# Kernel optimization log

Hardware: AMD Instinct MI355X
Metric: run time of the kernel (lower is better)

Reference implementation:

```python
import math
import jax, jax.numpy as jnp
import numpy as np

B, S, E = 4, 2048, 1024

def setup_inputs() -> dict:
    key = jax.random.key(0)
    k1, k2, k3 = jax.random.split(key, 3)
    X = jax.random.normal(k1, (B, S, E), dtype=jnp.float32)
    # nn.Linear(E, 3E): weight [3E, E], bias [3E]; scale weights for sane softmax
    W = jax.random.normal(k2, (3 * E, E), dtype=jnp.float32) * (1.0 / math.sqrt(E))
    b = jax.random.normal(k3, (3 * E,), dtype=jnp.float32) * 0.01
    return {"X": X, "W": W, "b": b}

def reference(X, W, b):
    E_ = X.shape[-1]
    # fused QKV projection: X @ W^T + b -> [B, S, 3E]
    qkv = jnp.einsum('bse,fe->bsf', X, W) + b
    q, k, v = jnp.split(qkv, 3, axis=-1)
    scores = jnp.einsum('bqe,bke->bqk', q, k) / math.sqrt(E_)
    attention_weight = jax.nn.softmax(scores, axis=-1)  # [B, S, S]
    output = jnp.einsum('bqk,bke->bqe', attention_weight, v)
    return (output, attention_weight)
```

## Files before the change

kernel.cpp:

```cpp
#include <hip/hip_runtime.h>
#include <math.h>

typedef __bf16 bf16;
typedef __bf16 bf16x4 __attribute__((ext_vector_type(4)));
typedef __bf16 bf16x8 __attribute__((ext_vector_type(8)));
typedef float f32x4 __attribute__((ext_vector_type(4)));

#define MODE_QKV    0
#define MODE_SCORES 1
#define MODE_PV     2

__device__ inline void gload_lds16(const bf16* g, bf16* l) {
    __builtin_amdgcn_global_load_lds(
        (const __attribute__((address_space(1))) void*)g,
        (__attribute__((address_space(3))) void*)l, 16, 0, 0);
}

template <int MODE>
__global__ __launch_bounds__(256) void mfma_nt(
    const bf16* __restrict__ A, const bf16* __restrict__ B,
    const float* __restrict__ bias, void* __restrict__ Cv,
    int K, int lda, int ldb, int ldc,
    long sA, long sB, long sC, float alpha)
{
    A += (long)blockIdx.z * sA;
    B += (long)blockIdx.z * sB;

    __shared__ bf16 As[128 * 32] __attribute__((aligned(16)));
    __shared__ bf16 Bs[128 * 32] __attribute__((aligned(16)));

    const int t  = threadIdx.x;
    const int m0 = blockIdx.y * 128;
    const int n0 = blockIdx.x * 128;

    const int lane = t & 63;
    const int wave = t >> 6;
    const int wrow = (wave >> 1) * 64;
    const int wcol = (wave & 1) * 64;
    const int fr   = lane & 15;
    const int kq8  = lane >> 4;

    const int r0 = t >> 2,         q0 = t & 3;
    const int r1 = (t + 256) >> 2, q1 = (t + 256) & 3;
    const int k80 = (q0 ^ ((r0 >> 1) & 3)) * 8;
    const int k81 = (q1 ^ ((r1 >> 1) & 3)) * 8;

    f32x4 acc[4][4] = {};

    for (int k0 = 0; k0 < K; k0 += 32) {
        gload_lds16(A + (long)(m0 + r0) * lda + k0 + k80, &As[t * 8]);
        gload_lds16(A + (long)(m0 + r1) * lda + k0 + k81, &As[(t + 256) * 8]);
        gload_lds16(B + (long)(n0 + r0) * ldb + k0 + k80, &Bs[t * 8]);
        gload_lds16(B + (long)(n0 + r1) * ldb + k0 + k81, &Bs[(t + 256) * 8]);
        __syncthreads();

        bf16x8 af[4], bfr[4];
#pragma unroll
        for (int i = 0; i < 4; i++) {
            const int ra = wrow + i * 16 + fr;
            const int rb = wcol + i * 16 + fr;
            af[i]  = *(const bf16x8*)&As[(ra * 4 + (kq8 ^ ((ra >> 1) & 3))) * 8];
            bfr[i] = *(const bf16x8*)&Bs[(rb * 4 + (kq8 ^ ((rb >> 1) & 3))) * 8];
        }
#pragma unroll
        for (int i = 0; i < 4; i++)
#pragma unroll
            for (int j = 0; j < 4; j++)
                acc[i][j] = __builtin_amdgcn_mfma_f32_16x16x32_bf16(
                    af[i], bfr[j], acc[i][j], 0, 0, 0);
        __syncthreads();
    }

    const int r4 = (lane >> 4) * 4;
    if constexpr (MODE == MODE_PV) {
        float* C = (float*)Cv + (long)blockIdx.z * sC;
#pragma unroll
        for (int j = 0; j < 4; j++) {
            const int col = n0 + wcol + j * 16 + fr;
#pragma unroll
            for (int i = 0; i < 4; i++)
#pragma unroll
                for (int r = 0; r < 4; r++) {
                    const long row = m0 + wrow + i * 16 + r4 + r;
                    C[row * ldc + col] = acc[i][j][r];
                }
        }
    } else {
        bf16* C = (bf16*)Cv + (long)blockIdx.z * sC;
#pragma unroll
        for (int j = 0; j < 4; j++) {
            const int col = n0 + wcol + j * 16 + fr;
            const float bv = (MODE == MODE_QKV) ? bias[col] : 0.f;
#pragma unroll
            for (int i = 0; i < 4; i++)
#pragma unroll
                for (int r = 0; r < 4; r++) {
                    const long row = m0 + wrow + i * 16 + r4 + r;
                    float v = acc[i][j][r];
                    if constexpr (MODE == MODE_QKV)
                        C[row * ldc + col] = (bf16)(v + bv);
                    else
                        C[row * ldc + col] = (bf16)__expf(alpha * v);
                }
        }
    }
}

__global__ __launch_bounds__(256) void f32_to_bf16(
    const float* __restrict__ in, bf16* __restrict__ out, long n)
{
    long i = ((long)blockIdx.x * 256 + threadIdx.x) * 4;
    if (i < n) {
        float4 v = *(const float4*)(in + i);
        bf16x4 o = { (bf16)v.x, (bf16)v.y, (bf16)v.z, (bf16)v.w };
        *(bf16x4*)(out + i) = o;
    }
}

__global__ __launch_bounds__(256) void transpose_v(
    const bf16* __restrict__ V, bf16* __restrict__ Vt)
{
    __shared__ bf16 tile[32][33];
    const bf16* Vb  = V  + (long)blockIdx.z * 2048 * 3072;
    bf16*       Vtb = Vt + (long)blockIdx.z * 1024 * 2048;
    const int s0 = blockIdx.x * 32, e0 = blockIdx.y * 32;
    const int tx = threadIdx.x & 31, ty = threadIdx.x >> 5;
#pragma unroll
    for (int i = 0; i < 32; i += 8)
        tile[ty + i][tx] = Vb[(long)(s0 + ty + i) * 3072 + e0 + tx];
    __syncthreads();
#pragma unroll
    for (int i = 0; i < 32; i += 8)
        Vtb[(long)(e0 + ty + i) * 2048 + s0 + tx] = tile[tx][ty + i];
}

__global__ __launch_bounds__(256) void norm_rows(
    bf16* __restrict__ Pu, float* __restrict__ out1)
{
    bf16* p  = Pu   + (long)blockIdx.x * 2048;
    float* o = out1 + (long)blockIdx.x * 2048;
    const int t = threadIdx.x;
    bf16x8 v = *(const bf16x8*)(p + t * 8);
    float f[8];
    float s = 0.f;
#pragma unroll
    for (int k = 0; k < 8; k++) { f[k] = (float)v[k]; s += f[k]; }
#pragma unroll
    for (int off = 32; off > 0; off >>= 1) s += __shfl_xor(s, off);
    __shared__ float red[4];
    const int wid = t >> 6, lane = t & 63;
    if (lane == 0) red[wid] = s;
    __syncthreads();
    s = red[0] + red[1] + red[2] + red[3];
    const float inv = 1.0f / s;
    float4 a, b;
    a.x = f[0] * inv; a.y = f[1] * inv; a.z = f[2] * inv; a.w = f[3] * inv;
    b.x = f[4] * inv; b.y = f[5] * inv; b.z = f[6] * inv; b.w = f[7] * inv;
    *(float4*)(o + t * 8)     = a;
    *(float4*)(o + t * 8 + 4) = b;
    bf16x8 w;
#pragma unroll
    for (int k = 0; k < 8; k++) w[k] = (bf16)(f[k] * inv);
    *(bf16x8*)(p + t * 8) = w;
}

extern "C" void kernel_launch(void* const* d_in, const int* in_sizes, int n_in,
                              void* d_out, int out_size, void* d_ws, size_t ws_size,
                              hipStream_t stream)
{
    const int B = 4, S = 2048, E = 1024;
    const float* X    = (const float*)d_in[0];
    const float* W    = (const float*)d_in[1];
    const float* bias = (const float*)d_in[2];

    float* out0 = (float*)d_out;
    float* out1 = out0 + (long)B * S * E;

    char* ws = (char*)d_ws;
    bf16* qkvb = (bf16*)(ws);
    bf16* Vt   = (bf16*)(ws + 50331648);
    bf16* Pu   = (bf16*)(ws + 67108864);
    bf16* Xb   = (bf16*)(ws + 67108864);
    bf16* Wb   = (bf16*)(ws + 83886080);

    f32_to_bf16<<<(long)B * S * E / 1024, 256, 0, stream>>>(X, Xb, (long)B * S * E);
    f32_to_bf16<<<(long)3 * E * E / 1024, 256, 0, stream>>>(W, Wb, (long)3 * E * E);

    mfma_nt<MODE_QKV><<<dim3(3 * E / 128, B * S / 128, 1), 256, 0, stream>>>(
        Xb, Wb, bias, qkvb, E, E, E, 3 * E, 0, 0, 0, 1.0f);

    transpose_v<<<dim3(S / 32, E / 32, B), 256, 0, stream>>>(qkvb + 2 * E, Vt);

    mfma_nt<MODE_SCORES><<<dim3(S / 128, S / 128, B), 256, 0, stream>>>(
        qkvb, qkvb + E, nullptr, Pu, E, 3 * E, 3 * E, S,
        (long)S * 3 * E, (long)S * 3 * E, (long)S * S, 0.03125f);

    norm_rows<<<B * S, 256, 0, stream>>>(Pu, out1);

    mfma_nt<MODE_PV><<<dim3(E / 128, S / 128, B), 256, 0, stream>>>(
        Pu, Vt, nullptr, out0, S, S, S, E,
        (long)S * S, (long)E * S, (long)S * E, 1.0f);
}
```

Baseline: 346.7 us.

## Rework GEMM kernel into 8-wave 256-row tiles with 4-stage LDS pipeline

Replaces the 4-wave 128x128 GEMM with an 8-wave kernel using 256-row tiles (256 or 128 columns) and a 4-deep ring of LDS buffers filled by async global-to-LDS loads issued three tiles ahead. Loads are interleaved with MFMA phases behind explicit vmcnt waits and barriers, and setprio raises wave priority during MFMA bursts. The aim is to hide global-memory latency and increase data reuse per tile. The cost is much more LDS and more accumulator registers per thread, which lowers occupancy and makes correctness depend on hand-tuned wait counts.

```diff
diff --git a/kernel.cpp b/kernel.cpp
--- a/kernel.cpp
+++ b/kernel.cpp
@@ -16,87 +16,154 @@
         (__attribute__((address_space(3))) void*)l, 16, 0, 0);
 }
 
-template <int MODE>
-__global__ __launch_bounds__(256) void mfma_nt(
+template <int MODE, int BN>
+__global__ __launch_bounds__(512) void mfma_nt8(
     const bf16* __restrict__ A, const bf16* __restrict__ B,
     const float* __restrict__ bias, void* __restrict__ Cv,
     int K, int lda, int ldb, int ldc,
     long sA, long sB, long sC, float alpha)
 {
+    constexpr int BM  = 256, BK = 32;
+    constexpr int WN  = BN / 4;
+    constexpr int NJ  = WN / 16;
+    constexpr int LB  = (BN == 256) ? 2 : 1;
+    constexpr int LPT = 2 + LB;
+
     A += (long)blockIdx.z * sA;
     B += (long)blockIdx.z * sB;
 
-    __shared__ bf16 As[128 * 32] __attribute__((aligned(16)));
-    __shared__ bf16 Bs[128 * 32] __attribute__((aligned(16)));
-
-    const int t  = threadIdx.x;
-    const int m0 = blockIdx.y * 128;
-    const int n0 = blockIdx.x * 128;
-
+    __shared__ bf16 As[4 * BM * BK] __attribute__((aligned(16)));
+    __shared__ bf16 Bs[4 * BN * BK] __attribute__((aligned(16)));
+
+    const int t    = threadIdx.x;
+    const int m0   = blockIdx.y * BM;
+    const int n0   = blockIdx.x * BN;
     const int lane = t & 63;
     const int wave = t >> 6;
-    const int wrow = (wave >> 1) * 64;
-    const int wcol = (wave & 1) * 64;
+    const int wr   = (wave >> 2) * 128;
+    const int wc   = (wave & 3) * WN;
     const int fr   = lane & 15;
     const int kq8  = lane >> 4;
 
-    const int r0 = t >> 2,         q0 = t & 3;
-    const int r1 = (t + 256) >> 2, q1 = (t + 256) & 3;
-    const int k80 = (q0 ^ ((r0 >> 1) & 3)) * 8;
-    const int k81 = (q1 ^ ((r1 >> 1) & 3)) * 8;
-
-    f32x4 acc[4][4] = {};
-
-    for (int k0 = 0; k0 < K; k0 += 32) {
-        gload_lds16(A + (long)(m0 + r0) * lda + k0 + k80, &As[t * 8]);
-        gload_lds16(A + (long)(m0 + r1) * lda + k0 + k81, &As[(t + 256) * 8]);
-        gload_lds16(B + (long)(n0 + r0) * ldb + k0 + k80, &Bs[t * 8]);
-        gload_lds16(B + (long)(n0 + r1) * ldb + k0 + k81, &Bs[(t + 256) * 8]);
-        __syncthreads();
-
-        bf16x8 af[4], bfr[4];
-#pragma unroll
-        for (int i = 0; i < 4; i++) {
-            const int ra = wrow + i * 16 + fr;
-            const int rb = wcol + i * 16 + fr;
-            af[i]  = *(const bf16x8*)&As[(ra * 4 + (kq8 ^ ((ra >> 1) & 3))) * 8];
-            bfr[i] = *(const bf16x8*)&Bs[(rb * 4 + (kq8 ^ ((rb >> 1) & 3))) * 8];
-        }
+    const int ra0 = t >> 2,         qa0 = t & 3;
+    const int ra1 = (t + 512) >> 2, qa1 = (t + 512) & 3;
+    const int ga0 = (qa0 ^ ((ra0 >> 1) & 3)) * 8;
+    const int ga1 = (qa1 ^ ((ra1 >> 1) & 3)) * 8;
+
+    const bf16* gA0 = A + (long)(m0 + ra0) * lda + ga0;
+    const bf16* gA1 = A + (long)(m0 + ra1) * lda + ga1;
+    const bf16* gB0 = B + (long)(n0 + ra0) * ldb + ga0;
+    const bf16* gB1 = B + (long)(n0 + ((LB == 2) ? ra1 : ra0)) * ldb
+                        + ((LB == 2) ? ga1 : ga0);
+
+    int offA[8], offB[NJ];
+#pragma unroll
+    for (int i = 0; i < 8; i++) {
+        const int r = wr + i * 16 + fr;
+        offA[i] = (r * 4 + (kq8 ^ ((r >> 1) & 3))) * 8;
+    }
+#pragma unroll
+    for (int j = 0; j < NJ; j++) {
+        const int r = wc + j * 16 + fr;
+        offB[j] = (r * 4 + (kq8 ^ ((r >> 1) & 3))) * 8;
+    }
+
+    const int NT = K / BK;
+
+#define STAGE_A(tt) do {                                                   \
+    const int  _s = (tt) & 3; const long _k = (long)(tt) * BK;             \
+    gload_lds16(gA0 + _k, &As[_s * BM * BK + t * 8]);                      \
+    gload_lds16(gA1 + _k, &As[_s * BM * BK + (t + 512) * 8]);              \
+} while (0)
+
+#define STAGE_B(tt) do {                                                   \
+    const int  _s = (tt) & 3; const long _k = (long)(tt) * BK;             \
+    gload_lds16(gB0 + _k, &Bs[_s * BN * BK + t * 8]);                      \
+    if constexpr (LB == 2)                                                 \
+        gload_lds16(gB1 + _k, &Bs[_s * BN * BK + (t + 512) * 8]);          \
+} while (0)
+
+    f32x4 acc[8][NJ] = {};
+
+    STAGE_A(0); STAGE_B(0);
+    STAGE_A(1); STAGE_B(1);
+    STAGE_A(2); STAGE_B(2);
+    asm volatile("s_waitcnt vmcnt(%0)" :: "i"(2 * LPT) : "memory");
+    __builtin_amdgcn_s_barrier();
+
+    for (int tt = 0; tt < NT; ++tt) {
+        const bf16* as = &As[(tt & 3) * BM * BK];
+        const bf16* bs = &Bs[(tt & 3) * BN * BK];
+        bf16x8 af[4], bfr[NJ];
+
+        if (tt + 3 < NT) STAGE_A(tt + 3);
+#pragma unroll
+        for (int i = 0; i < 4; i++) af[i] = *(const bf16x8*)&as[offA[i]];
+#pragma unroll
+        for (int j = 0; j < NJ; j++) bfr[j] = *(const bf16x8*)&bs[offB[j]];
+        asm volatile("" ::: "memory");
+        __builtin_amdgcn_s_barrier();
+        __builtin_amdgcn_s_setprio(1);
 #pragma unroll
         for (int i = 0; i < 4; i++)
 #pragma unroll
-            for (int j = 0; j < 4; j++)
+            for (int j = 0; j < NJ; j++)
                 acc[i][j] = __builtin_amdgcn_mfma_f32_16x16x32_bf16(
                     af[i], bfr[j], acc[i][j], 0, 0, 0);
-        __syncthreads();
-    }
+        __builtin_amdgcn_s_setprio(0);
+        asm volatile("" ::: "memory");
+        __builtin_amdgcn_s_barrier();
+
+        if (tt + 3 < NT) STAGE_B(tt + 3);
+#pragma unroll
+        for (int i = 0; i < 4; i++) af[i] = *(const bf16x8*)&as[offA[4 + i]];
+        asm volatile("" ::: "memory");
+        __builtin_amdgcn_s_barrier();
+        __builtin_amdgcn_s_setprio(1);
+#pragma unroll
+        for (int i = 0; i < 4; i++)
+#pragma unroll
+            for (int j = 0; j < NJ; j++)
+                acc[4 + i][j] = __builtin_amdgcn_mfma_f32_16x16x32_bf16(
+                    af[i], bfr[j], acc[4 + i][j], 0, 0, 0);
+        __builtin_amdgcn_s_setprio(0);
+        if (tt < NT - 3)
+            asm volatile("s_waitcnt vmcnt(%0)" :: "i"(2 * LPT) : "memory");
+        else if (tt == NT - 3)
+            asm volatile("s_waitcnt vmcnt(%0)" :: "i"(LPT) : "memory");
+        else if (tt == NT - 2)
+            asm volatile("s_waitcnt vmcnt(0)" ::: "memory");
+        __builtin_amdgcn_s_barrier();
+    }
+#undef STAGE_A
+#undef STAGE_B
 
     const int r4 = (lane >> 4) * 4;
     if constexpr (MODE == MODE_PV) {
         float* C = (float*)Cv + (long)blockIdx.z * sC;
 #pragma unroll
-        for (int j = 0; j < 4; j++) {
-            const int col = n0 + wcol + j * 16 + fr;
-#pragma unroll
-            for (int i = 0; i < 4; i++)
+        for (int j = 0; j < NJ; j++) {
+            const int col = n0 + wc + j * 16 + fr;
+#pragma unroll
+            for (int I = 0; I < 8; I++)
 #pragma unroll
                 for (int r = 0; r < 4; r++) {
-                    const long row = m0 + wrow + i * 16 + r4 + r;
-                    C[row * ldc + col] = acc[i][j][r];
+                    const long row = m0 + wr + I * 16 + r4 + r;
+                    C[row * ldc + col] = acc[I][j][r];
                 }
         }
     } else {
         bf16* C = (bf16*)Cv + (long)blockIdx.z * sC;
 #pragma unroll
-        for (int j = 0; j < 4; j++) {
-            const int col = n0 + wcol + j * 16 + fr;
+        for (int j = 0; j < NJ; j++) {
+            const int col = n0 + wc + j * 16 + fr;
             const float bv = (MODE == MODE_QKV) ? bias[col] : 0.f;
 #pragma unroll
-            for (int i = 0; i < 4; i++)
+            for (int I = 0; I < 8; I++)
 #pragma unroll
                 for (int r = 0; r < 4; r++) {
-                    const long row = m0 + wrow + i * 16 + r4 + r;
-                    float v = acc[i][j][r];
+                    const long row = m0 + wr + I * 16 + r4 + r;
+                    float v = acc[I][j][r];
                     if constexpr (MODE == MODE_QKV)
                         C[row * ldc + col] = (bf16)(v + bv);
                     else
@@ -186,18 +253,18 @@
     f32_to_bf16<<<(long)B * S * E / 1024, 256, 0, stream>>>(X, Xb, (long)B * S * E);
     f32_to_bf16<<<(long)3 * E * E / 1024, 256, 0, stream>>>(W, Wb, (long)3 * E * E);
 
-    mfma_nt<MODE_QKV><<<dim3(3 * E / 128, B * S / 128, 1), 256, 0, stream>>>(
+    mfma_nt8<MODE_QKV, 128><<<dim3(3 * E / 128, B * S / 256, 1), 512, 0, stream>>>(
         Xb, Wb, bias, qkvb, E, E, E, 3 * E, 0, 0, 0, 1.0f);
 
     transpose_v<<<dim3(S / 32, E / 32, B), 256, 0, stream>>>(qkvb + 2 * E, Vt);
 
-    mfma_nt<MODE_SCORES><<<dim3(S / 128, S / 128, B), 256, 0, stream>>>(
+    mfma_nt8<MODE_SCORES, 256><<<dim3(S / 256, S / 256, B), 512, 0, stream>>>(
         qkvb, qkvb + E, nullptr, Pu, E, 3 * E, 3 * E, S,
         (long)S * 3 * E, (long)S * 3 * E, (long)S * S, 0.03125f);
 
     norm_rows<<<B * S, 256, 0, stream>>>(Pu, out1);
 
-    mfma_nt<MODE_PV><<<dim3(E / 128, S / 128, B), 256, 0, stream>>>(
+    mfma_nt8<MODE_PV, 128><<<dim3(E / 128, S / 256, B), 512, 0, stream>>>(
         Pu, Vt, nullptr, out0, S, S, S, E,
         (long)S * S, (long)E * S, (long)S * E, 1.0f);
 }
```

Result: slower. 362.0 us (+4.4%).

## Triple-buffer GEMM LDS tiles with async prefetch and split MFMA waits

Applied to the files above, without the earlier changes.

Replaces the single-buffered load, sync, compute loop in the shared GEMM kernel with a three-slot LDS ring. Tile k+2 is prefetched via global_load_lds while tile k is computed, with explicit vmcnt/lgkmcnt waits and one barrier per iteration. LDS reads are issued as inline ds_read_b128 and the MFMAs are split into two halves, so the first half can start before all fragments arrive. Wave priority is raised around the MFMA blocks. The cost is three times the LDS per block, which may lower occupancy, and correctness now relies on hand-placed waitcnt values that the compiler does not check.

```diff
diff --git a/kernel.cpp b/kernel.cpp
--- a/kernel.cpp
+++ b/kernel.cpp
@@ -14,6 +14,14 @@
     __builtin_amdgcn_global_load_lds(
         (const __attribute__((address_space(1))) void*)g,
         (__attribute__((address_space(3))) void*)l, 16, 0, 0);
+}
+
+__device__ inline bf16x8 ds_read16(const bf16* p) {
+    bf16x8 r;
+    asm volatile("ds_read_b128 %0, %1"
+        : "=v"(r)
+        : "v"((const __attribute__((address_space(3))) bf16*)p));
+    return r;
 }
 
 template <int MODE>
@@ -23,11 +31,13 @@
     int K, int lda, int ldb, int ldc,
     long sA, long sB, long sC, float alpha)
 {
+    constexpr int SLOT = 128 * 32;
+
     A += (long)blockIdx.z * sA;
     B += (long)blockIdx.z * sB;
 
-    __shared__ bf16 As[128 * 32] __attribute__((aligned(16)));
-    __shared__ bf16 Bs[128 * 32] __attribute__((aligned(16)));
+    __shared__ bf16 As[3 * SLOT] __attribute__((aligned(16)));
+    __shared__ bf16 Bs[3 * SLOT] __attribute__((aligned(16)));
 
     const int t  = threadIdx.x;
     const int m0 = blockIdx.y * 128;
@@ -45,31 +55,88 @@
     const int k80 = (q0 ^ ((r0 >> 1) & 3)) * 8;
     const int k81 = (q1 ^ ((r1 >> 1) & 3)) * 8;
 
+    const bf16* gA0 = A + (long)(m0 + r0) * lda + k80;
+    const bf16* gA1 = A + (long)(m0 + r1) * lda + k81;
+    const bf16* gB0 = B + (long)(n0 + r0) * ldb + k80;
+    const bf16* gB1 = B + (long)(n0 + r1) * ldb + k81;
+
+    int offA[4], offB[4];
+#pragma unroll
+    for (int i = 0; i < 4; i++) {
+        const int ra = wrow + i * 16 + fr;
+        const int rb = wcol + i * 16 + fr;
+        offA[i] = (ra * 4 + (kq8 ^ ((ra >> 1) & 3))) * 8;
+        offB[i] = (rb * 4 + (kq8 ^ ((rb >> 1) & 3))) * 8;
+    }
+
+    const int NT = K / 32;
+
+#define STAGE(tt_, ss_) do {                                               \
+    const long _k = (long)(tt_) * 32;                                      \
+    bf16* _as = &As[(ss_) * SLOT];                                         \
+    bf16* _bs = &Bs[(ss_) * SLOT];                                         \
+    gload_lds16(gA0 + _k, _as + t * 8);                                    \
+    gload_lds16(gA1 + _k, _as + (t + 256) * 8);                            \
+    gload_lds16(gB0 + _k, _bs + t * 8);                                    \
+    gload_lds16(gB1 + _k, _bs + (t + 256) * 8);                            \
+} while (0)
+
     f32x4 acc[4][4] = {};
 
-    for (int k0 = 0; k0 < K; k0 += 32) {
-        gload_lds16(A + (long)(m0 + r0) * lda + k0 + k80, &As[t * 8]);
-        gload_lds16(A + (long)(m0 + r1) * lda + k0 + k81, &As[(t + 256) * 8]);
-        gload_lds16(B + (long)(n0 + r0) * ldb + k0 + k80, &Bs[t * 8]);
-        gload_lds16(B + (long)(n0 + r1) * ldb + k0 + k81, &Bs[(t + 256) * 8]);
-        __syncthreads();
+    STAGE(0, 0);
+    STAGE(1, 1);
+    asm volatile("s_waitcnt vmcnt(4)" ::: "memory");
+    __builtin_amdgcn_s_barrier();
+
+    int cs = 0;
+    for (int tt = 0; tt < NT; ++tt) {
+        const int ss = (cs >= 1) ? cs - 1 : 2;
+        if (tt + 2 < NT) STAGE(tt + 2, ss);
+
+        const bf16* as = &As[cs * SLOT];
+        const bf16* bs = &Bs[cs * SLOT];
 
         bf16x8 af[4], bfr[4];
-#pragma unroll
-        for (int i = 0; i < 4; i++) {
-            const int ra = wrow + i * 16 + fr;
-            const int rb = wcol + i * 16 + fr;
-            af[i]  = *(const bf16x8*)&As[(ra * 4 + (kq8 ^ ((ra >> 1) & 3))) * 8];
-            bfr[i] = *(const bf16x8*)&Bs[(rb * 4 + (kq8 ^ ((rb >> 1) & 3))) * 8];
-        }
-#pragma unroll
-        for (int i = 0; i < 4; i++)
+        af[0]  = ds_read16(as + offA[0]);
+        af[1]  = ds_read16(as + offA[1]);
+        bfr[0] = ds_read16(bs + offB[0]);
+        bfr[1] = ds_read16(bs + offB[1]);
+        bfr[2] = ds_read16(bs + offB[2]);
+        bfr[3] = ds_read16(bs + offB[3]);
+        af[2]  = ds_read16(as + offA[2]);
+        af[3]  = ds_read16(as + offA[3]);
+
+        asm volatile("s_waitcnt lgkmcnt(2)" ::: "memory");
+        __builtin_amdgcn_sched_barrier(0);
+        __builtin_amdgcn_s_setprio(1);
+#pragma unroll
+        for (int i = 0; i < 2; i++)
 #pragma unroll
             for (int j = 0; j < 4; j++)
                 acc[i][j] = __builtin_amdgcn_mfma_f32_16x16x32_bf16(
                     af[i], bfr[j], acc[i][j], 0, 0, 0);
-        __syncthreads();
-    }
+        __builtin_amdgcn_s_setprio(0);
+
+        asm volatile("s_waitcnt lgkmcnt(0)" ::: "memory");
+        __builtin_amdgcn_sched_barrier(0);
+        __builtin_amdgcn_s_setprio(1);
+#pragma unroll
+        for (int i = 2; i < 4; i++)
+#pragma unroll
+            for (int j = 0; j < 4; j++)
+                acc[i][j] = __builtin_amdgcn_mfma_f32_16x16x32_bf16(
+                    af[i], bfr[j], acc[i][j], 0, 0, 0);
+        __builtin_amdgcn_s_setprio(0);
+
+        if (tt + 2 < NT)
+            asm volatile("s_waitcnt vmcnt(4)" ::: "memory");
+        else
+            asm volatile("s_waitcnt vmcnt(0)" ::: "memory");
+        __builtin_amdgcn_s_barrier();
+
+        cs = (cs < 2) ? cs + 1 : 0;
+    }
+#undef STAGE
 
     const int r4 = (lane >> 4) * 4;
     if constexpr (MODE == MODE_PV) {
```

New measurement: 312.3 us. 1.11x faster.

## Enlarge GEMM tiles to 256x128 with triple-buffered async LDS pipeline

Applied to the files above, without the earlier changes.

The shared MFMA GEMM kernel now computes a 256x128 tile per block, giving each wave 128x64 and more reuse per LDS load. It keeps three LDS stages, issues global-to-LDS loads two k-tiles ahead, and splits each iteration into four MFMA phases with s_setprio and barriers. This is meant to hide global load latency behind compute and cut the per-k-step sync overhead of the single-buffered loop. In exchange it uses more LDS (72KB) and registers, which limits occupancy, and halves the number of blocks, which may hurt load balance on the smaller GEMMs.

```diff
diff --git a/kernel.cpp b/kernel.cpp
--- a/kernel.cpp
+++ b/kernel.cpp
@@ -16,72 +16,177 @@
         (__attribute__((address_space(3))) void*)l, 16, 0, 0);
 }
 
+__device__ inline bf16x8 ds_read16(const bf16* p) {
+    bf16x8 r;
+    asm volatile("ds_read_b128 %0, %1"
+        : "=v"(r)
+        : "v"((const __attribute__((address_space(3))) bf16*)p));
+    return r;
+}
+
 template <int MODE>
-__global__ __launch_bounds__(256) void mfma_nt(
+__global__ __launch_bounds__(256, 2) void mfma_nt(
     const bf16* __restrict__ A, const bf16* __restrict__ B,
     const float* __restrict__ bias, void* __restrict__ Cv,
     int K, int lda, int ldb, int ldc,
     long sA, long sB, long sC, float alpha)
 {
+    constexpr int ASLOT = 256 * 32;
+    constexpr int BSLOT = 128 * 32;
+
     A += (long)blockIdx.z * sA;
     B += (long)blockIdx.z * sB;
 
-    __shared__ bf16 As[128 * 32] __attribute__((aligned(16)));
-    __shared__ bf16 Bs[128 * 32] __attribute__((aligned(16)));
+    __shared__ bf16 As[3 * ASLOT] __attribute__((aligned(16)));
+    __shared__ bf16 Bs[3 * BSLOT] __attribute__((aligned(16)));
 
     const int t  = threadIdx.x;
-    const int m0 = blockIdx.y * 128;
+    const int m0 = blockIdx.y * 256;
     const int n0 = blockIdx.x * 128;
 
     const int lane = t & 63;
     const int wave = t >> 6;
-    const int wrow = (wave >> 1) * 64;
-    const int wcol = (wave & 1) * 64;
+    const int wr   = (wave >> 1) * 128;
+    const int wc   = (wave & 1) * 64;
     const int fr   = lane & 15;
     const int kq8  = lane >> 4;
 
-    const int r0 = t >> 2,         q0 = t & 3;
-    const int r1 = (t + 256) >> 2, q1 = (t + 256) & 3;
-    const int k80 = (q0 ^ ((r0 >> 1) & 3)) * 8;
-    const int k81 = (q1 ^ ((r1 >> 1) & 3)) * 8;
-
-    f32x4 acc[4][4] = {};
-
-    for (int k0 = 0; k0 < K; k0 += 32) {
-        gload_lds16(A + (long)(m0 + r0) * lda + k0 + k80, &As[t * 8]);
-        gload_lds16(A + (long)(m0 + r1) * lda + k0 + k81, &As[(t + 256) * 8]);
-        gload_lds16(B + (long)(n0 + r0) * ldb + k0 + k80, &Bs[t * 8]);
-        gload_lds16(B + (long)(n0 + r1) * ldb + k0 + k81, &Bs[(t + 256) * 8]);
-        __syncthreads();
-
-        bf16x8 af[4], bfr[4];
-#pragma unroll
-        for (int i = 0; i < 4; i++) {
-            const int ra = wrow + i * 16 + fr;
-            const int rb = wcol + i * 16 + fr;
-            af[i]  = *(const bf16x8*)&As[(ra * 4 + (kq8 ^ ((ra >> 1) & 3))) * 8];
-            bfr[i] = *(const bf16x8*)&Bs[(rb * 4 + (kq8 ^ ((rb >> 1) & 3))) * 8];
-        }
+    const bf16* gA[4];
+    const bf16* gB[2];
+#pragma unroll
+    for (int l = 0; l < 4; l++) {
+        const int c = t + 256 * l;
+        const int r = c >> 2;
+        const int k8 = ((c & 3) ^ ((r >> 1) & 3)) * 8;
+        gA[l] = A + (long)(m0 + r) * lda + k8;
+    }
+#pragma unroll
+    for (int l = 0; l < 2; l++) {
+        const int c = t + 256 * l;
+        const int r = c >> 2;
+        const int k8 = ((c & 3) ^ ((r >> 1) & 3)) * 8;
+        gB[l] = B + (long)(n0 + r) * ldb + k8;
+    }
+
+    int offA[8], offB[4];
+#pragma unroll
+    for (int i = 0; i < 8; i++) {
+        const int r = wr + i * 16 + fr;
+        offA[i] = (r * 4 + (kq8 ^ ((r >> 1) & 3))) * 8;
+    }
+#pragma unroll
+    for (int j = 0; j < 4; j++) {
+        const int r = wc + j * 16 + fr;
+        offB[j] = (r * 4 + (kq8 ^ ((r >> 1) & 3))) * 8;
+    }
+
+    const int NT = K / 32;
+
+#define STA(l, ss_, tt_) \
+    gload_lds16(gA[l] + (long)(tt_) * 32, &As[(ss_) * ASLOT + (t + 256 * (l)) * 8])
+#define STB(l, ss_, tt_) \
+    gload_lds16(gB[l] + (long)(tt_) * 32, &Bs[(ss_) * BSLOT + (t + 256 * (l)) * 8])
+
+    f32x4 acc[8][4] = {};
+
+    STA(0,0,0); STA(1,0,0); STA(2,0,0); STA(3,0,0); STB(0,0,0); STB(1,0,0);
+    STA(0,1,1); STA(1,1,1); STA(2,1,1); STA(3,1,1); STB(0,1,1); STB(1,1,1);
+    asm volatile("s_waitcnt vmcnt(6)" ::: "memory");
+    __builtin_amdgcn_s_barrier();
+
+    int cs = 0;
+    for (int tt = 0; tt < NT; ++tt) {
+        const int ss = (cs >= 1) ? cs - 1 : 2;
+        const bool st = (tt + 2 < NT);
+        const bf16* as = &As[cs * ASLOT];
+        const bf16* bs = &Bs[cs * BSLOT];
+
+        bf16x8 af[8], bq[4];
+
+        if (st) { STA(0, ss, tt + 2); STA(1, ss, tt + 2); }
+        af[0] = ds_read16(as + offA[0]);
+        af[1] = ds_read16(as + offA[1]);
+        af[2] = ds_read16(as + offA[2]);
+        af[3] = ds_read16(as + offA[3]);
+        bq[0] = ds_read16(bs + offB[0]);
+        bq[1] = ds_read16(bs + offB[1]);
+        __builtin_amdgcn_s_barrier();
+        asm volatile("s_waitcnt lgkmcnt(0)" ::: "memory");
+        __builtin_amdgcn_sched_barrier(0);
+        __builtin_amdgcn_s_setprio(1);
 #pragma unroll
         for (int i = 0; i < 4; i++)
 #pragma unroll
-            for (int j = 0; j < 4; j++)
+            for (int j = 0; j < 2; j++)
                 acc[i][j] = __builtin_amdgcn_mfma_f32_16x16x32_bf16(
-                    af[i], bfr[j], acc[i][j], 0, 0, 0);
-        __syncthreads();
-    }
+                    af[i], bq[j], acc[i][j], 0, 0, 0);
+        __builtin_amdgcn_s_setprio(0);
+
+        if (st) { STA(2, ss, tt + 2); STA(3, ss, tt + 2); }
+        bq[2] = ds_read16(bs + offB[2]);
+        bq[3] = ds_read16(bs + offB[3]);
+        __builtin_amdgcn_s_barrier();
+        asm volatile("s_waitcnt lgkmcnt(0)" ::: "memory");
+        __builtin_amdgcn_sched_barrier(0);
+        __builtin_amdgcn_s_setprio(1);
+#pragma unroll
+        for (int i = 0; i < 4; i++)
+#pragma unroll
+            for (int j = 2; j < 4; j++)
+                acc[i][j] = __builtin_amdgcn_mfma_f32_16x16x32_bf16(
+                    af[i], bq[j], acc[i][j], 0, 0, 0);
+        __builtin_amdgcn_s_setprio(0);
+
+        if (st) { STB(0, ss, tt + 2); }
+        af[4] = ds_read16(as + offA[4]);
+        af[5] = ds_read16(as + offA[5]);
+        af[6] = ds_read16(as + offA[6]);
+        af[7] = ds_read16(as + offA[7]);
+        __builtin_amdgcn_s_barrier();
+        asm volatile("s_waitcnt lgkmcnt(0)" ::: "memory");
+        __builtin_amdgcn_sched_barrier(0);
+        __builtin_amdgcn_s_setprio(1);
+#pragma unroll
+        for (int i = 4; i < 8; i++)
+#pragma unroll
+            for (int j = 0; j < 2; j++)
+                acc[i][j] = __builtin_amdgcn_mfma_f32_16x16x32_bf16(
+                    af[i], bq[j], acc[i][j], 0, 0, 0);
+        __builtin_amdgcn_s_setprio(0);
+
+        if (st) { STB(1, ss, tt + 2); }
+        __builtin_amdgcn_s_barrier();
+        __builtin_amdgcn_s_setprio(1);
+#pragma unroll
+        for (int i = 4; i < 8; i++)
+#pragma unroll
+            for (int j = 2; j < 4; j++)
+                acc[i][j] = __builtin_amdgcn_mfma_f32_16x16x32_bf16(
+                    af[i], bq[j], acc[i][j], 0, 0, 0);
+        __builtin_amdgcn_s_setprio(0);
+
+        if (st)
+            asm volatile("s_waitcnt vmcnt(6)" ::: "memory");
+        else
+            asm volatile("s_waitcnt vmcnt(0)" ::: "memory");
+        __builtin_amdgcn_s_barrier();
+
+        cs = (cs < 2) ? cs + 1 : 0;
+    }
+#undef STA
+#undef STB
 
     const int r4 = (lane >> 4) * 4;
     if constexpr (MODE == MODE_PV) {
         float* C = (float*)Cv + (long)blockIdx.z * sC;
 #pragma unroll
         for (int j = 0; j < 4; j++) {
-            const int col = n0 + wcol + j * 16 + fr;
-#pragma unroll
-            for (int i = 0; i < 4; i++)
+            const int col = n0 + wc + j * 16 + fr;
+#pragma unroll
+            for (int i = 0; i < 8; i++)
 #pragma unroll
                 for (int r = 0; r < 4; r++) {
-                    const long row = m0 + wrow + i * 16 + r4 + r;
+                    const long row = m0 + wr + i * 16 + r4 + r;
                     C[row * ldc + col] = acc[i][j][r];
                 }
         }
@@ -89,13 +194,13 @@
         bf16* C = (bf16*)Cv + (long)blockIdx.z * sC;
 #pragma unroll
         for (int j = 0; j < 4; j++) {
-            const int col = n0 + wcol + j * 16 + fr;
+            const int col = n0 + wc + j * 16 + fr;
             const float bv = (MODE == MODE_QKV) ? bias[col] : 0.f;
 #pragma unroll
-            for (int i = 0; i < 4; i++)
+            for (int i = 0; i < 8; i++)
 #pragma unroll
                 for (int r = 0; r < 4; r++) {
-                    const long row = m0 + wrow + i * 16 + r4 + r;
+                    const long row = m0 + wr + i * 16 + r4 + r;
                     float v = acc[i][j][r];
                     if constexpr (MODE == MODE_QKV)
                         C[row * ldc + col] = (bf16)(v + bv);
@@ -186,18 +291,18 @@
     f32_to_bf16<<<(long)B * S * E / 1024, 256, 0, stream>>>(X, Xb, (long)B * S * E);
     f32_to_bf16<<<(long)3 * E * E / 1024, 256, 0, stream>>>(W, Wb, (long)3 * E * E);
 
-    mfma_nt<MODE_QKV><<<dim3(3 * E / 128, B * S / 128, 1), 256, 0, stream>>>(
+    mfma_nt<MODE_QKV><<<dim3(3 * E / 128, B * S / 256, 1), 256, 0, stream>>>(
         Xb, Wb, bias, qkvb, E, E, E, 3 * E, 0, 0, 0, 1.0f);
 
     transpose_v<<<dim3(S / 32, E / 32, B), 256, 0, stream>>>(qkvb + 2 * E, Vt);
 
-    mfma_nt<MODE_SCORES><<<dim3(S / 128, S / 128, B), 256, 0, stream>>>(
+    mfma_nt<MODE_SCORES><<<dim3(S / 128, S / 256, B), 256, 0, stream>>>(
         qkvb, qkvb + E, nullptr, Pu, E, 3 * E, 3 * E, S,
         (long)S * 3 * E, (long)S * 3 * E, (long)S * S, 0.03125f);
 
     norm_rows<<<B * S, 256, 0, stream>>>(Pu, out1);
 
-    mfma_nt<MODE_PV><<<dim3(E / 128, S / 128, B), 256, 0, stream>>>(
+    mfma_nt<MODE_PV><<<dim3(E / 128, S / 256, B), 256, 0, stream>>>(
         Pu, Vt, nullptr, out0, S, S, S, E,
         (long)S * S, (long)E * S, (long)S * E, 1.0f);
 }
```

Result: faster. 314.3 us (-9.3%).
